# Optimization experiments

Measured on AMD Instinct MI355X. Metric: run time of the kernel, lower is better.

## Reference

```python
import jax, jax.numpy as jnp
import numpy as np
import math

N_HEAD = 16

def setup_inputs() -> dict:
    key = jax.random.key(0)
    k1, k2, k3, k4, k5 = jax.random.split(key, 5)
    B, T, C = 8, 1024, 1024
    scale = 0.02
    return {
        "x": jax.random.normal(k1, (B, T, C), dtype=jnp.float32),
        "w_attn": jax.random.normal(k2, (C, 3 * C), dtype=jnp.float32) * scale,
        "b_attn": jax.random.normal(k3, (3 * C,), dtype=jnp.float32) * scale,
        "w_proj": jax.random.normal(k4, (C, C), dtype=jnp.float32) * scale,
        "b_proj": jax.random.normal(k5, (C,), dtype=jnp.float32) * scale,
    }

def reference(x, w_attn, b_attn, w_proj, b_proj):
    B, T, C = x.shape
    H = N_HEAD
    hd = C // H
    # QKV projection: [B,T,3C]
    qkv = jnp.einsum("btc,cd->btd", x, w_attn) + b_attn
    q, k, v = jnp.split(qkv, 3, axis=-1)
    # [B,T,C] -> [B,H,T,hd]
    def heads(t):
        return t.reshape(B, T, H, hd).transpose(0, 2, 1, 3)
    q, k, v = heads(q), heads(k), heads(v)
    # scaled QK^T: [B,H,T,T]
    att = jnp.einsum("bhqd,bhkd->bhqk", q, k) * (1.0 / math.sqrt(hd))
    # causal mask (tril of block_size cropped to T)
    causal = jnp.tril(jnp.ones((T, T), dtype=bool))
    att = jnp.where(causal, att, jnp.float32(-jnp.inf))
    att = jax.nn.softmax(att, axis=-1)
    # attention-weighted values: [B,H,T,hd] -> [B,T,C]
    y = jnp.einsum("bhqk,bhkd->bhqd", att, v)
    y = y.transpose(0, 2, 1, 3).reshape(B, T, C)
    # output projection
    return jnp.einsum("btc,cd->btd", y, w_proj) + b_proj
```

## Files before the change

kernel.cpp:

```cpp
#include <hip/hip_runtime.h>

typedef __bf16 bf16x8 __attribute__((ext_vector_type(8)));
typedef float f32x4 __attribute__((ext_vector_type(4)));
typedef unsigned short u16;
typedef unsigned int u32;

__device__ __forceinline__ u16 f2bf(float f) {
  u32 u = __builtin_bit_cast(u32, f);
  u32 r = (u + 0x7FFFu + ((u >> 16) & 1u)) >> 16;
  return (u16)r;
}

__device__ __forceinline__ void gload_lds16(const u16* g, u16* l) {
  __builtin_amdgcn_global_load_lds(
      (const __attribute__((address_space(1))) u32*)g,
      (__attribute__((address_space(3))) u32*)l, 16, 0, 0);
}

__global__ void cast_x_kernel(const float* __restrict__ in, u16* __restrict__ out, int n4) {
  int i = blockIdx.x * blockDim.x + threadIdx.x;
  if (i >= n4) return;
  float4 v = ((const float4*)in)[i];
  uint2 o;
  o.x = (u32)f2bf(v.x) | ((u32)f2bf(v.y) << 16);
  o.y = (u32)f2bf(v.z) | ((u32)f2bf(v.w) << 16);
  ((uint2*)out)[i] = o;
}

__global__ void transpose_cast_kernel(const float* __restrict__ in, u16* __restrict__ out,
                                      int K, int N) {
  __shared__ float tile[32][33];
  int n0 = blockIdx.x * 32, k0 = blockIdx.y * 32;
  int tx = threadIdx.x & 31, ty = threadIdx.x >> 5;
#pragma unroll
  for (int i = 0; i < 32; i += 8)
    tile[ty + i][tx] = in[(size_t)(k0 + ty + i) * N + n0 + tx];
  __syncthreads();
#pragma unroll
  for (int i = 0; i < 32; i += 8)
    out[(size_t)(n0 + ty + i) * K + k0 + tx] = f2bf(tile[tx][ty + i]);
}

template <int MODE>
__global__ __launch_bounds__(256, 3) void gemm_bf16(
    const u16* __restrict__ A, const u16* __restrict__ Bt,
    const float* __restrict__ bias, u16* __restrict__ out_q,
    float* __restrict__ out_f, int M, int N, int K) {
  __shared__ alignas(16) u16 As[128 * 64];
  __shared__ alignas(16) u16 Bs[128 * 64];
  const int tiles_n = N >> 7;
  const int bid0 = blockIdx.x;
  const int cpx = (int)gridDim.x >> 3;
  const int swz = (bid0 & 7) * cpx + (bid0 >> 3);
  const int tm = swz / tiles_n;
  const int tn = swz % tiles_n;
  const int tid = threadIdx.x;
  const int wave = tid >> 6, lane = tid & 63;
  const int wr = (wave >> 1) * 64, wc = (wave & 1) * 64;
  const int lr = lane & 15, lg = lane >> 4;

  f32x4 acc[4][4] = {};
  const size_t a_base = (size_t)(tm * 128) * K;
  const size_t b_base = (size_t)(tn * 128) * K;

  for (int k0 = 0; k0 < K; k0 += 64) {
#pragma unroll
    for (int i = 0; i < 4; ++i) {
      int c = i * 256 + tid;
      int row = c >> 3, ch = c & 7;
      int sw = (ch ^ (row & 7)) * 8;
      gload_lds16(A + a_base + (size_t)row * K + k0 + sw, &As[c * 8]);
      gload_lds16(Bt + b_base + (size_t)row * K + k0 + sw, &Bs[c * 8]);
    }
    __syncthreads();
    bf16x8 af[4][2], bfr[4][2];
#pragma unroll
    for (int m = 0; m < 4; ++m) {
      int row = wr + m * 16 + lr;
#pragma unroll
      for (int kk = 0; kk < 2; ++kk)
        af[m][kk] = *(const bf16x8*)&As[(row * 64 + kk * 32 + lg * 8) ^ ((row & 7) << 3)];
    }
#pragma unroll
    for (int n = 0; n < 4; ++n) {
      int row = wc + n * 16 + lr;
#pragma unroll
      for (int kk = 0; kk < 2; ++kk)
        bfr[n][kk] = *(const bf16x8*)&Bs[(row * 64 + kk * 32 + lg * 8) ^ ((row & 7) << 3)];
    }
#pragma unroll
    for (int m = 0; m < 4; ++m)
#pragma unroll
      for (int n = 0; n < 4; ++n) {
        if constexpr (MODE == 0) {
          acc[m][n] = __builtin_amdgcn_mfma_f32_16x16x32_bf16(bfr[n][0], af[m][0], acc[m][n], 0, 0, 0);
          acc[m][n] = __builtin_amdgcn_mfma_f32_16x16x32_bf16(bfr[n][1], af[m][1], acc[m][n], 0, 0, 0);
        } else {
          acc[m][n] = __builtin_amdgcn_mfma_f32_16x16x32_bf16(af[m][0], bfr[n][0], acc[m][n], 0, 0, 0);
          acc[m][n] = __builtin_amdgcn_mfma_f32_16x16x32_bf16(af[m][1], bfr[n][1], acc[m][n], 0, 0, 0);
        }
      }
    __syncthreads();
  }

  if constexpr (MODE == 0) {
    const int tok0 = tm * 128 + wr;
    const int col0 = tn * 128 + wc;
#pragma unroll
    for (int n = 0; n < 4; ++n) {
      int ncol = col0 + n * 16 + lg * 4;
      float4 bv = *(const float4*)&bias[ncol];
      int which = ncol >> 10, c = ncol & 1023;
      int h = c >> 6, d = c & 63;
#pragma unroll
      for (int m = 0; m < 4; ++m) {
        int tok = tok0 + m * 16 + lr;
        int b = tok >> 10, t = tok & 1023;
        union { u16 s[4]; uint2 v; } pk;
        pk.s[0] = f2bf(acc[m][n][0] + bv.x);
        pk.s[1] = f2bf(acc[m][n][1] + bv.y);
        pk.s[2] = f2bf(acc[m][n][2] + bv.z);
        pk.s[3] = f2bf(acc[m][n][3] + bv.w);
        *(uint2*)&out_q[(size_t)which * 8388608 + ((((size_t)b * 16 + h) * 1024 + t) << 6) + d] = pk.v;
      }
    }
  } else {
    const int row0 = tm * 128 + wr;
    const int col0 = tn * 128 + wc;
#pragma unroll
    for (int n = 0; n < 4; ++n) {
      int col = col0 + n * 16 + lr;
      float bv = bias[col];
#pragma unroll
      for (int m = 0; m < 4; ++m)
#pragma unroll
        for (int r = 0; r < 4; ++r) {
          int mrow = row0 + m * 16 + lg * 4 + r;
          out_f[(size_t)mrow * N + col] = acc[m][n][r] + bv;
        }
    }
  }
}

__global__ __launch_bounds__(256, 2) void attn_kernel(
    const u16* __restrict__ Qb, const u16* __restrict__ Kb,
    const u16* __restrict__ Vb, u16* __restrict__ yb) {
  __shared__ alignas(16) u16 Ks[128 * 64];
  __shared__ alignas(16) u16 Vt[64 * 128];
  __shared__ alignas(16) u16 Pl[4][32 * 128];
  __shared__ float abuf[4][32];

  const int bid = blockIdx.x;
  const int xcd = bid & 7, j = bid >> 3;
  const int bh = ((j >> 2) << 3) + xcd;
  const int pr = j & 3;
  const size_t hb = (size_t)bh * 65536;
  const int tid = threadIdx.x, w = tid >> 6, lane = tid & 63;
  const int lr = lane & 15, lg = lane >> 4;
  const int b = bh >> 4, h = bh & 15;

  for (int pass = 0; pass < 2; ++pass) {
    const int qt = pass ? (7 - pr) : pr;
    const int q0 = qt * 128 + w * 32;

    bf16x8 qf[2][2];
#pragma unroll
    for (int mi = 0; mi < 2; ++mi)
#pragma unroll
      for (int ks = 0; ks < 2; ++ks)
        qf[mi][ks] = *(const bf16x8*)&Qb[hb + (size_t)(q0 + mi * 16 + lr) * 64 + ks * 32 + lg * 8];

    float m_run[2] = {-1e30f, -1e30f}, l_run[2] = {0.f, 0.f};
    f32x4 o[2][4] = {};

    const int nkt = qt + 1;
    for (int kt = 0; kt < nkt; ++kt) {
#pragma unroll
      for (int i = 0; i < 4; ++i) {
        int c = i * 256 + tid;
        int row = c >> 3, ch = c & 7;
        gload_lds16(Kb + hb + (size_t)(kt * 128 + row) * 64 + ((ch ^ (row & 7)) * 8), &Ks[c * 8]);
      }
      {
        int key = tid & 127, d0 = (tid >> 7) * 32;
        const u16* src = Vb + hb + (size_t)(kt * 128 + key) * 64 + d0;
        union { uint4 v[4]; u16 s[32]; } tmp;
        tmp.v[0] = *(const uint4*)src;
        tmp.v[1] = *(const uint4*)(src + 8);
        tmp.v[2] = *(const uint4*)(src + 16);
        tmp.v[3] = *(const uint4*)(src + 24);
#pragma unroll
        for (int jj = 0; jj < 32; ++jj) {
          int d = d0 + jj;
          Vt[d * 128 + (key ^ ((d & 7) << 3))] = tmp.s[jj];
        }
      }
      __syncthreads();

      {
        f32x4 s[8][2] = {};
        __builtin_amdgcn_s_setprio(1);
#pragma unroll
        for (int ni = 0; ni < 8; ++ni) {
          int krow = ni * 16 + lr;
          bf16x8 kf0 = *(const bf16x8*)&Ks[(krow * 64 + lg * 8) ^ ((krow & 7) << 3)];
          bf16x8 kf1 = *(const bf16x8*)&Ks[(krow * 64 + 32 + lg * 8) ^ ((krow & 7) << 3)];
#pragma unroll
          for (int mi = 0; mi < 2; ++mi) {
            s[ni][mi] = __builtin_amdgcn_mfma_f32_16x16x32_bf16(kf0, qf[mi][0], s[ni][mi], 0, 0, 0);
            s[ni][mi] = __builtin_amdgcn_mfma_f32_16x16x32_bf16(kf1, qf[mi][1], s[ni][mi], 0, 0, 0);
          }
        }
        __builtin_amdgcn_s_setprio(0);

        const bool need_mask = (kt == qt);
        float alpha_l[2];
#pragma unroll
        for (int mi = 0; mi < 2; ++mi) {
          float v = -1e30f;
#pragma unroll
          for (int ni = 0; ni < 8; ++ni)
#pragma unroll
            for (int r = 0; r < 4; ++r) {
              float sv = s[ni][mi][r];
              if (need_mask) {
                int ka = kt * 128 + ni * 16 + lg * 4 + r;
                int qa = q0 + mi * 16 + lr;
                if (ka > qa) sv = -1e30f;
              }
              s[ni][mi][r] = sv;
              v = fmaxf(v, sv);
            }
          v = fmaxf(v, __shfl_xor(v, 16));
          v = fmaxf(v, __shfl_xor(v, 32));
          float mn = fmaxf(m_run[mi], v);
          float al = __expf((m_run[mi] - mn) * 0.125f);
          m_run[mi] = mn;
          float mh = mn * 0.125f;
          float rs = 0.f;
#pragma unroll
          for (int ni = 0; ni < 8; ++ni)
#pragma unroll
            for (int r = 0; r < 4; ++r) {
              float p = __expf(s[ni][mi][r] * 0.125f - mh);
              s[ni][mi][r] = p;
              rs += p;
            }
          rs += __shfl_xor(rs, 16);
          rs += __shfl_xor(rs, 32);
          l_run[mi] = l_run[mi] * al + rs;
          alpha_l[mi] = al;
        }
        if (lg == 0) {
          abuf[w][lr] = alpha_l[0];
          abuf[w][16 + lr] = alpha_l[1];
        }
#pragma unroll
        for (int mi = 0; mi < 2; ++mi) {
          int qrow = mi * 16 + lr;
          u16* dst = &Pl[w][qrow * 128];
          int sw = (qrow & 7) << 3;
#pragma unroll
          for (int ni = 0; ni < 8; ++ni)
#pragma unroll
            for (int r = 0; r < 4; ++r)
              dst[(ni * 16 + lg * 4 + r) ^ sw] = f2bf(s[ni][mi][r]);
        }
        asm volatile("s_waitcnt lgkmcnt(0)" ::: "memory");
#pragma unroll
        for (int mi = 0; mi < 2; ++mi) {
          f32x4 av;
#pragma unroll
          for (int r = 0; r < 4; ++r) av[r] = abuf[w][mi * 16 + lg * 4 + r];
#pragma unroll
          for (int nd = 0; nd < 4; ++nd)
#pragma unroll
            for (int r = 0; r < 4; ++r) o[mi][nd][r] *= av[r];
        }
        __builtin_amdgcn_s_setprio(1);
#pragma unroll
        for (int ks = 0; ks < 4; ++ks) {
          bf16x8 pf[2];
#pragma unroll
          for (int mi = 0; mi < 2; ++mi) {
            int prow = mi * 16 + lr;
            pf[mi] = *(const bf16x8*)&Pl[w][prow * 128 + (((ks * 4 + lg) ^ (prow & 7)) * 8)];
          }
#pragma unroll
          for (int nd = 0; nd < 4; ++nd) {
            int vrow = nd * 16 + lr;
            bf16x8 vf = *(const bf16x8*)&Vt[vrow * 128 + (((ks * 4 + lg) ^ (vrow & 7)) * 8)];
#pragma unroll
            for (int mi = 0; mi < 2; ++mi)
              o[mi][nd] = __builtin_amdgcn_mfma_f32_16x16x32_bf16(pf[mi], vf, o[mi][nd], 0, 0, 0);
          }
        }
        __builtin_amdgcn_s_setprio(0);
      }
      __syncthreads();
    }

    if (lg == 0) {
      abuf[w][lr] = l_run[0];
      abuf[w][16 + lr] = l_run[1];
    }
    asm volatile("s_waitcnt lgkmcnt(0)" ::: "memory");
#pragma unroll
    for (int mi = 0; mi < 2; ++mi) {
      f32x4 inv;
#pragma unroll
      for (int r = 0; r < 4; ++r) inv[r] = 1.f / abuf[w][mi * 16 + lg * 4 + r];
#pragma unroll
      for (int nd = 0; nd < 4; ++nd)
#pragma unroll
        for (int r = 0; r < 4; ++r) {
          int t = q0 + mi * 16 + lg * 4 + r;
          int c = h * 64 + nd * 16 + lr;
          yb[((size_t)b * 1024 + t) * 1024 + c] = f2bf(o[mi][nd][r] * inv[r]);
        }
    }
    __syncthreads();
  }
}

extern "C" void kernel_launch(void* const* d_in, const int* in_sizes, int n_in,
                              void* d_out, int out_size, void* d_ws, size_t ws_size,
                              hipStream_t stream) {
  const float* x = (const float*)d_in[0];
  const float* w_attn = (const float*)d_in[1];
  const float* b_attn = (const float*)d_in[2];
  const float* w_proj = (const float*)d_in[3];
  const float* b_proj = (const float*)d_in[4];
  float* out = (float*)d_out;

  u16* ws = (u16*)d_ws;
  u16* xb = ws;
  u16* watT = xb + 8388608;
  u16* wpT = watT + 3145728;
  u16* Qb = wpT + 1048576;
  u16* yb = xb;

  cast_x_kernel<<<8192, 256, 0, stream>>>(x, xb, 2097152);
  {
    dim3 g(96, 32);
    transpose_cast_kernel<<<g, 256, 0, stream>>>(w_attn, watT, 1024, 3072);
  }
  {
    dim3 g(32, 32);
    transpose_cast_kernel<<<g, 256, 0, stream>>>(w_proj, wpT, 1024, 1024);
  }
  gemm_bf16<0><<<64 * 24, 256, 0, stream>>>(xb, watT, b_attn, Qb, nullptr, 8192, 3072, 1024);
  attn_kernel<<<512, 256, 0, stream>>>(Qb, Qb + 8388608, Qb + 2 * 8388608, yb);
  gemm_bf16<1><<<64 * 8, 256, 0, stream>>>(yb, wpT, b_proj, nullptr, out, 8192, 1024, 1024);
}
```

Before: 169.5 us.

## Store V pre-transposed from QKV GEMM and streamline attention softmax

The QKV GEMM epilogue now writes V in a transposed [b,h,d,t] layout, so the attention kernel loads V tiles straight into LDS with async global_load_lds instead of doing a scalar register transpose. The attention kernel halves the P staging buffer by processing keys in two halves, and uses exp2 with a prescaled constant. It packs bf16 with v_cvt_pk_bf16_f32, broadcasts alpha and l with shuffles instead of LDS round trips, and raises the occupancy target to 3. In exchange, the GEMM's V stores become strided scalar 2-byte writes, and the extra LDS wait per half adds synchronisation.

```diff
diff --git a/kernel.cpp b/kernel.cpp
--- a/kernel.cpp
+++ b/kernel.cpp
@@ -4,6 +4,7 @@
 typedef float f32x4 __attribute__((ext_vector_type(4)));
 typedef unsigned short u16;
 typedef unsigned int u32;
+typedef unsigned long long u64;
 
 __device__ __forceinline__ u16 f2bf(float f) {
   u32 u = __builtin_bit_cast(u32, f);
@@ -116,12 +117,20 @@
       for (int m = 0; m < 4; ++m) {
         int tok = tok0 + m * 16 + lr;
         int b = tok >> 10, t = tok & 1023;
-        union { u16 s[4]; uint2 v; } pk;
-        pk.s[0] = f2bf(acc[m][n][0] + bv.x);
-        pk.s[1] = f2bf(acc[m][n][1] + bv.y);
-        pk.s[2] = f2bf(acc[m][n][2] + bv.z);
-        pk.s[3] = f2bf(acc[m][n][3] + bv.w);
-        *(uint2*)&out_q[(size_t)which * 8388608 + ((((size_t)b * 16 + h) * 1024 + t) << 6) + d] = pk.v;
+        if (which < 2) {
+          union { u16 s[4]; uint2 v; } pk;
+          pk.s[0] = f2bf(acc[m][n][0] + bv.x);
+          pk.s[1] = f2bf(acc[m][n][1] + bv.y);
+          pk.s[2] = f2bf(acc[m][n][2] + bv.z);
+          pk.s[3] = f2bf(acc[m][n][3] + bv.w);
+          *(uint2*)&out_q[(size_t)which * 8388608 + ((((size_t)b * 16 + h) * 1024 + t) << 6) + d] = pk.v;
+        } else {
+          size_t base = (size_t)2 * 8388608 + (((size_t)b * 16 + h) * 64 + d) * 1024 + t;
+          out_q[base] = f2bf(acc[m][n][0] + bv.x);
+          out_q[base + 1024] = f2bf(acc[m][n][1] + bv.y);
+          out_q[base + 2048] = f2bf(acc[m][n][2] + bv.z);
+          out_q[base + 3072] = f2bf(acc[m][n][3] + bv.w);
+        }
       }
     }
   } else {
@@ -142,13 +151,12 @@
   }
 }
 
-__global__ __launch_bounds__(256, 2) void attn_kernel(
+__global__ __launch_bounds__(256, 3) void attn_kernel(
     const u16* __restrict__ Qb, const u16* __restrict__ Kb,
     const u16* __restrict__ Vb, u16* __restrict__ yb) {
   __shared__ alignas(16) u16 Ks[128 * 64];
   __shared__ alignas(16) u16 Vt[64 * 128];
-  __shared__ alignas(16) u16 Pl[4][32 * 128];
-  __shared__ float abuf[4][32];
+  __shared__ alignas(16) u16 Pl[4][32 * 64];
 
   const int bid = blockIdx.x;
   const int xcd = bid & 7, j = bid >> 3;
@@ -158,6 +166,7 @@
   const int tid = threadIdx.x, w = tid >> 6, lane = tid & 63;
   const int lr = lane & 15, lg = lane >> 4;
   const int b = bh >> 4, h = bh & 15;
+  const float C2 = 0.18033688011112042f;
 
   for (int pass = 0; pass < 2; ++pass) {
     const int qt = pass ? (7 - pr) : pr;
@@ -181,115 +190,111 @@
         int row = c >> 3, ch = c & 7;
         gload_lds16(Kb + hb + (size_t)(kt * 128 + row) * 64 + ((ch ^ (row & 7)) * 8), &Ks[c * 8]);
       }
-      {
-        int key = tid & 127, d0 = (tid >> 7) * 32;
-        const u16* src = Vb + hb + (size_t)(kt * 128 + key) * 64 + d0;
-        union { uint4 v[4]; u16 s[32]; } tmp;
-        tmp.v[0] = *(const uint4*)src;
-        tmp.v[1] = *(const uint4*)(src + 8);
-        tmp.v[2] = *(const uint4*)(src + 16);
-        tmp.v[3] = *(const uint4*)(src + 24);
-#pragma unroll
-        for (int jj = 0; jj < 32; ++jj) {
-          int d = d0 + jj;
-          Vt[d * 128 + (key ^ ((d & 7) << 3))] = tmp.s[jj];
-        }
+#pragma unroll
+      for (int i = 0; i < 4; ++i) {
+        int c = i * 256 + tid;
+        int row = c >> 4, ch = c & 15;
+        gload_lds16(Vb + hb + (size_t)row * 1024 + kt * 128 + ((ch ^ (row & 15)) * 8), &Vt[c * 8]);
       }
       __syncthreads();
 
-      {
-        f32x4 s[8][2] = {};
-        __builtin_amdgcn_s_setprio(1);
+      f32x4 s[8][2] = {};
+      __builtin_amdgcn_s_setprio(1);
+#pragma unroll
+      for (int ni = 0; ni < 8; ++ni) {
+        int krow = ni * 16 + lr;
+        bf16x8 kf0 = *(const bf16x8*)&Ks[(krow * 64 + lg * 8) ^ ((krow & 7) << 3)];
+        bf16x8 kf1 = *(const bf16x8*)&Ks[(krow * 64 + 32 + lg * 8) ^ ((krow & 7) << 3)];
+#pragma unroll
+        for (int mi = 0; mi < 2; ++mi) {
+          s[ni][mi] = __builtin_amdgcn_mfma_f32_16x16x32_bf16(kf0, qf[mi][0], s[ni][mi], 0, 0, 0);
+          s[ni][mi] = __builtin_amdgcn_mfma_f32_16x16x32_bf16(kf1, qf[mi][1], s[ni][mi], 0, 0, 0);
+        }
+      }
+      __builtin_amdgcn_s_setprio(0);
+
+      const bool need_mask = (kt == qt);
+      float alpha_l[2];
+#pragma unroll
+      for (int mi = 0; mi < 2; ++mi) {
+        if (need_mask) {
+#pragma unroll
+          for (int ni = 0; ni < 8; ++ni)
+#pragma unroll
+            for (int r = 0; r < 4; ++r) {
+              int ka = kt * 128 + ni * 16 + lg * 4 + r;
+              int qa = q0 + mi * 16 + lr;
+              if (ka > qa) s[ni][mi][r] = -1e30f;
+            }
+        }
+        float pm[8];
+#pragma unroll
+        for (int ni = 0; ni < 8; ++ni)
+          pm[ni] = fmaxf(fmaxf(s[ni][mi][0], s[ni][mi][1]), fmaxf(s[ni][mi][2], s[ni][mi][3]));
+        float v = fmaxf(fmaxf(fmaxf(pm[0], pm[1]), fmaxf(pm[2], pm[3])),
+                        fmaxf(fmaxf(pm[4], pm[5]), fmaxf(pm[6], pm[7])));
+        v = fmaxf(v, __shfl_xor(v, 16));
+        v = fmaxf(v, __shfl_xor(v, 32));
+        float mn = fmaxf(m_run[mi], v);
+        float mc = mn * C2;
+        float al = __builtin_amdgcn_exp2f(m_run[mi] * C2 - mc);
+        m_run[mi] = mn;
+        float ps[8];
 #pragma unroll
         for (int ni = 0; ni < 8; ++ni) {
-          int krow = ni * 16 + lr;
-          bf16x8 kf0 = *(const bf16x8*)&Ks[(krow * 64 + lg * 8) ^ ((krow & 7) << 3)];
-          bf16x8 kf1 = *(const bf16x8*)&Ks[(krow * 64 + 32 + lg * 8) ^ ((krow & 7) << 3)];
-#pragma unroll
-          for (int mi = 0; mi < 2; ++mi) {
-            s[ni][mi] = __builtin_amdgcn_mfma_f32_16x16x32_bf16(kf0, qf[mi][0], s[ni][mi], 0, 0, 0);
-            s[ni][mi] = __builtin_amdgcn_mfma_f32_16x16x32_bf16(kf1, qf[mi][1], s[ni][mi], 0, 0, 0);
-          }
-        }
-        __builtin_amdgcn_s_setprio(0);
-
-        const bool need_mask = (kt == qt);
-        float alpha_l[2];
-#pragma unroll
-        for (int mi = 0; mi < 2; ++mi) {
-          float v = -1e30f;
-#pragma unroll
-          for (int ni = 0; ni < 8; ++ni)
-#pragma unroll
-            for (int r = 0; r < 4; ++r) {
-              float sv = s[ni][mi][r];
-              if (need_mask) {
-                int ka = kt * 128 + ni * 16 + lg * 4 + r;
-                int qa = q0 + mi * 16 + lr;
-                if (ka > qa) sv = -1e30f;
-              }
-              s[ni][mi][r] = sv;
-              v = fmaxf(v, sv);
-            }
-          v = fmaxf(v, __shfl_xor(v, 16));
-          v = fmaxf(v, __shfl_xor(v, 32));
-          float mn = fmaxf(m_run[mi], v);
-          float al = __expf((m_run[mi] - mn) * 0.125f);
-          m_run[mi] = mn;
-          float mh = mn * 0.125f;
-          float rs = 0.f;
-#pragma unroll
-          for (int ni = 0; ni < 8; ++ni)
-#pragma unroll
-            for (int r = 0; r < 4; ++r) {
-              float p = __expf(s[ni][mi][r] * 0.125f - mh);
-              s[ni][mi][r] = p;
-              rs += p;
-            }
-          rs += __shfl_xor(rs, 16);
-          rs += __shfl_xor(rs, 32);
-          l_run[mi] = l_run[mi] * al + rs;
-          alpha_l[mi] = al;
-        }
-        if (lg == 0) {
-          abuf[w][lr] = alpha_l[0];
-          abuf[w][16 + lr] = alpha_l[1];
-        }
+#pragma unroll
+          for (int r = 0; r < 4; ++r)
+            s[ni][mi][r] = __builtin_amdgcn_exp2f(fmaf(s[ni][mi][r], C2, -mc));
+          ps[ni] = (s[ni][mi][0] + s[ni][mi][1]) + (s[ni][mi][2] + s[ni][mi][3]);
+        }
+        float rs = ((ps[0] + ps[1]) + (ps[2] + ps[3])) + ((ps[4] + ps[5]) + (ps[6] + ps[7]));
+        rs += __shfl_xor(rs, 16);
+        rs += __shfl_xor(rs, 32);
+        l_run[mi] = l_run[mi] * al + rs;
+        alpha_l[mi] = al;
+      }
+#pragma unroll
+      for (int mi = 0; mi < 2; ++mi) {
+        f32x4 av;
+#pragma unroll
+        for (int r = 0; r < 4; ++r) av[r] = __shfl(alpha_l[mi], lg * 4 + r);
+#pragma unroll
+        for (int nd = 0; nd < 4; ++nd)
+#pragma unroll
+          for (int r = 0; r < 4; ++r) o[mi][nd][r] *= av[r];
+      }
+#pragma unroll
+      for (int hh = 0; hh < 2; ++hh) {
 #pragma unroll
         for (int mi = 0; mi < 2; ++mi) {
           int qrow = mi * 16 + lr;
-          u16* dst = &Pl[w][qrow * 128];
           int sw = (qrow & 7) << 3;
 #pragma unroll
-          for (int ni = 0; ni < 8; ++ni)
-#pragma unroll
-            for (int r = 0; r < 4; ++r)
-              dst[(ni * 16 + lg * 4 + r) ^ sw] = f2bf(s[ni][mi][r]);
+          for (int nq = 0; nq < 4; ++nq) {
+            int ni = hh * 4 + nq;
+            u32 plo, phi;
+            asm("v_cvt_pk_bf16_f32 %0, %1, %2" : "=v"(plo) : "v"(s[ni][mi][0]), "v"(s[ni][mi][1]));
+            asm("v_cvt_pk_bf16_f32 %0, %1, %2" : "=v"(phi) : "v"(s[ni][mi][2]), "v"(s[ni][mi][3]));
+            u64 pv = (u64)plo | ((u64)phi << 32);
+            int e = (qrow * 64 + nq * 16 + lg * 4) ^ sw;
+            *(u64*)&Pl[w][e] = pv;
+          }
         }
         asm volatile("s_waitcnt lgkmcnt(0)" ::: "memory");
-#pragma unroll
-        for (int mi = 0; mi < 2; ++mi) {
-          f32x4 av;
-#pragma unroll
-          for (int r = 0; r < 4; ++r) av[r] = abuf[w][mi * 16 + lg * 4 + r];
-#pragma unroll
-          for (int nd = 0; nd < 4; ++nd)
-#pragma unroll
-            for (int r = 0; r < 4; ++r) o[mi][nd][r] *= av[r];
-        }
         __builtin_amdgcn_s_setprio(1);
 #pragma unroll
-        for (int ks = 0; ks < 4; ++ks) {
+        for (int kh = 0; kh < 2; ++kh) {
+          int ks = hh * 2 + kh;
           bf16x8 pf[2];
 #pragma unroll
           for (int mi = 0; mi < 2; ++mi) {
             int prow = mi * 16 + lr;
-            pf[mi] = *(const bf16x8*)&Pl[w][prow * 128 + (((ks * 4 + lg) ^ (prow & 7)) * 8)];
+            pf[mi] = *(const bf16x8*)&Pl[w][(prow * 64 + kh * 32 + lg * 8) ^ ((prow & 7) << 3)];
           }
 #pragma unroll
           for (int nd = 0; nd < 4; ++nd) {
             int vrow = nd * 16 + lr;
-            bf16x8 vf = *(const bf16x8*)&Vt[vrow * 128 + (((ks * 4 + lg) ^ (vrow & 7)) * 8)];
+            bf16x8 vf = *(const bf16x8*)&Vt[(vrow * 128 + ks * 32 + lg * 8) ^ ((vrow & 15) << 3)];
 #pragma unroll
             for (int mi = 0; mi < 2; ++mi)
               o[mi][nd] = __builtin_amdgcn_mfma_f32_16x16x32_bf16(pf[mi], vf, o[mi][nd], 0, 0, 0);
@@ -300,16 +305,11 @@
       __syncthreads();
     }
 
-    if (lg == 0) {
-      abuf[w][lr] = l_run[0];
-      abuf[w][16 + lr] = l_run[1];
-    }
-    asm volatile("s_waitcnt lgkmcnt(0)" ::: "memory");
 #pragma unroll
     for (int mi = 0; mi < 2; ++mi) {
       f32x4 inv;
 #pragma unroll
-      for (int r = 0; r < 4; ++r) inv[r] = 1.f / abuf[w][mi * 16 + lg * 4 + r];
+      for (int r = 0; r < 4; ++r) inv[r] = 1.f / __shfl(l_run[mi], lg * 4 + r);
 #pragma unroll
       for (int nd = 0; nd < 4; ++nd)
 #pragma unroll
```

New measurement: 262.0 us. +54.5%, slower.
